# Kernel tuning notes

Measured on AMD Instinct MI355X. Metric: run time of the kernel, lower is better.

The kernel has to match this reference:

```python
import jax, jax.numpy as jnp
import numpy as np

D_IN = 1024
D_OUT = 1024
NUM_HEADS = 16
HEAD_DIM = D_OUT // NUM_HEADS


def setup_inputs() -> dict:
    key = jax.random.key(0)
    ks = jax.random.split(key, 6)
    B, S = 2, 2048
    scale = 1.0 / np.sqrt(D_IN)
    x = jax.random.normal(ks[0], (B, S, D_IN), dtype=jnp.float32)
    # Linear weights stored torch-style as [out_features, in_features]
    Wq = jax.random.normal(ks[1], (D_OUT, D_IN), dtype=jnp.float32) * scale
    Wk = jax.random.normal(ks[2], (D_OUT, D_IN), dtype=jnp.float32) * scale
    Wv = jax.random.normal(ks[3], (D_OUT, D_IN), dtype=jnp.float32) * scale
    Wo = jax.random.normal(ks[4], (D_OUT, D_IN), dtype=jnp.float32) * scale
    bo = jax.random.normal(ks[5], (D_OUT,), dtype=jnp.float32) * 0.01
    return {"x": x, "Wq": Wq, "Wk": Wk, "Wv": Wv, "Wo": Wo, "bo": bo}


def reference(x, Wq, Wk, Wv, Wo, bo):
    B, S, _ = x.shape
    H, hd = NUM_HEADS, HEAD_DIM
    # QKV projections (qkv_bias=False), split into heads: [B, H, S, hd]
    q = (x @ Wq.T).reshape(B, S, H, hd).transpose(0, 2, 1, 3)
    k = (x @ Wk.T).reshape(B, S, H, hd).transpose(0, 2, 1, 3)
    v = (x @ Wv.T).reshape(B, S, H, hd).transpose(0, 2, 1, 3)
    # scaled causal attention scores [B, H, S, S]
    scores = jnp.einsum("bhqd,bhkd->bhqk", q, k) / jnp.sqrt(jnp.float32(hd))
    causal = jnp.tril(jnp.ones((S, S), dtype=bool))
    scores = jnp.where(causal, scores, jnp.finfo(scores.dtype).min)
    attn = jax.nn.softmax(scores, axis=-1)  # dropout p=0.0 -> identity
    ctx = jnp.einsum("bhqk,bhkd->bhqd", attn, v)  # [B, H, S, hd]
    ctx = ctx.transpose(0, 2, 1, 3).reshape(B, S, H * hd)
    return ctx @ Wo.T + bo
```

## Files before the change

kernel.cpp:

```cpp
#include <hip/hip_runtime.h>
#include <hip/hip_bf16.h>

#define AS1 __attribute__((address_space(1)))
#define AS3 __attribute__((address_space(3)))

typedef __attribute__((ext_vector_type(4))) float floatx4;
typedef __attribute__((ext_vector_type(8))) short bf16x8;
typedef unsigned short u16;
typedef unsigned int u32;

__device__ __forceinline__ u16 f2b(float f) {
  u32 u = __builtin_bit_cast(u32, f);
  u += 0x7fffu + ((u >> 16) & 1u);
  return (u16)(u >> 16);
}
__device__ __forceinline__ u32 pk2(float lo, float hi) {
  __hip_bfloat162 h = __float22bfloat162_rn(float2{lo, hi});
  u32 u;
  __builtin_memcpy(&u, &h, 4);
  return u;
}
__device__ __forceinline__ bf16x8 cvt8(float4 a, float4 b) {
  uint4 u{pk2(a.x, a.y), pk2(a.z, a.w), pk2(b.x, b.y), pk2(b.z, b.w)};
  return __builtin_bit_cast(bf16x8, u);
}

__device__ __forceinline__ void gld16(const void* g, AS3 u32* l) {
  __builtin_amdgcn_global_load_lds((const AS1 u32*)(const AS1 void*)g, l, 16,
                                   0, 0);
}

#define QSCALE 0.18033688011112042f
#define QSHIFT 14.4269504088896f

__global__ __launch_bounds__(256) void cvt_all(
    const float* __restrict__ x, const float* __restrict__ wq,
    const float* __restrict__ wk, const float* __restrict__ wv,
    const float* __restrict__ wo, u16* __restrict__ xb, u16* __restrict__ wqb,
    u16* __restrict__ wkb, u16* __restrict__ wvb, u16* __restrict__ wob) {
  const int i = blockIdx.x * 256 + threadIdx.x;
  const float* src;
  u16* dst;
  int off;
  if (i < 524288) {
    src = x; dst = xb; off = i;
  } else {
    const int j = i - 524288;
    const int wsel = j >> 17;
    off = j & 131071;
    src = (wsel == 0) ? wq : (wsel == 1) ? wk : (wsel == 2) ? wv : wo;
    dst = (wsel == 0) ? wqb : (wsel == 1) ? wkb : (wsel == 2) ? wvb : wob;
  }
  const float4* p = (const float4*)(src + (size_t)off * 8);
  *(bf16x8*)(dst + (size_t)off * 8) = cvt8(p[0], p[1]);
}

__device__ __forceinline__ void gemm_bf16(const u16* __restrict__ A,
                                          const u16* __restrict__ B, short* sA,
                                          short* sB, floatx4 acc[4][4]) {
  const int tid = threadIdx.x;
  const int lane = tid & 63;
  const int w = tid >> 6;
  const int l15 = lane & 15, quad = lane >> 4;
  const int wm = w >> 1, wn = w & 1;

  const u16* ga = A + ((size_t)(w * 32 + (lane >> 2))) * 1024 + (lane & 3) * 8;
  const u16* gb = B + ((size_t)(w * 32 + (lane >> 2))) * 1024 + (lane & 3) * 8;
  AS3 u32* la = (AS3 u32*)(AS3 short*)sA + w * 512;
  AS3 u32* lb = (AS3 u32*)(AS3 short*)sB + w * 512;

  for (int kt = 0; kt < 32; ++kt) {
    __syncthreads();
    gld16(ga, la);
    gld16(ga + (size_t)16 * 1024, la + 256);
    gld16(gb, lb);
    gld16(gb + (size_t)16 * 1024, lb + 256);
    ga += 32;
    gb += 32;
    __syncthreads();

    bf16x8 af[4], bfr[4];
#pragma unroll
    for (int mc = 0; mc < 4; ++mc)
      af[mc] = *(const bf16x8*)&sA[(wm * 64 + mc * 16 + l15) * 32 + quad * 8];
#pragma unroll
    for (int nc = 0; nc < 4; ++nc)
      bfr[nc] = *(const bf16x8*)&sB[(wn * 64 + nc * 16 + l15) * 32 + quad * 8];
#pragma unroll
    for (int mc = 0; mc < 4; ++mc)
#pragma unroll
      for (int nc = 0; nc < 4; ++nc)
        acc[mc][nc] = __builtin_amdgcn_mfma_f32_16x16x32_bf16(
            af[mc], bfr[nc], acc[mc][nc], 0, 0, 0);
  }
}

__device__ __forceinline__ void qkv_epilogue(floatx4 acc[4][4], int m0, int nb,
                                             int sel, u16* __restrict__ Q,
                                             u16* __restrict__ K,
                                             u16* __restrict__ Vt) {
  const int tid = threadIdx.x;
  const int lane = tid & 63, w = tid >> 6;
  const int l15 = lane & 15, quad = lane >> 4;
  const int wm = w >> 1, wn = w & 1;
#pragma unroll
  for (int mc = 0; mc < 4; ++mc) {
#pragma unroll
    for (int nc = 0; nc < 4; ++nc) {
      const int nn = nb + wn * 64 + nc * 16 + l15;
      const int h = nn >> 6, d = nn & 63;
#pragma unroll
      for (int r = 0; r < 4; ++r) {
        const int m = m0 + wm * 64 + mc * 16 + quad * 4 + r;
        const int b = m >> 11, s = m & 2047;
        const int bh = b * 16 + h;
        float av = acc[mc][nc][r];
        if (sel == 0) av *= QSCALE;
        const u16 v = f2b(av);
        if (sel == 0)
          Q[((size_t)bh * 2048 + s) * 64 + d] = v;
        else if (sel == 1)
          K[((size_t)bh * 2048 + s) * 64 + d] = v;
        else
          Vt[((size_t)bh * 64 + d) * 2048 + s] = v;
      }
    }
  }
}

__global__ __launch_bounds__(256) void qkv_gemm_b(
    const u16* __restrict__ xb, const u16* __restrict__ Wqb,
    const u16* __restrict__ Wkb, const u16* __restrict__ Wvb,
    u16* __restrict__ Q, u16* __restrict__ K, u16* __restrict__ Vt) {
  __shared__ __align__(16) short smem[2 * 128 * 32];
  const int m0 = blockIdx.x * 128;
  const int by = blockIdx.y;
  const int sel = by >> 3;
  const int nb = (by & 7) * 128;
  const u16* W = (sel == 0) ? Wqb : (sel == 1) ? Wkb : Wvb;

  floatx4 acc[4][4];
#pragma unroll
  for (int i = 0; i < 4; i++)
#pragma unroll
    for (int j = 0; j < 4; j++) acc[i][j] = (floatx4)0.0f;
  gemm_bf16(xb + (size_t)m0 * 1024, W + (size_t)nb * 1024, smem,
            smem + 128 * 32, acc);
  qkv_epilogue(acc, m0, nb, sel, Q, K, Vt);
}

__global__ __launch_bounds__(256) void out_gemm_b(const u16* __restrict__ ctx,
                                                  const u16* __restrict__ Wob,
                                                  const float* __restrict__ bo,
                                                  float* __restrict__ out) {
  __shared__ __align__(16) short smem[128 * 32 + 64 * 32];
  const int tid = threadIdx.x;
  const int lane = tid & 63, w = tid >> 6;
  const int l15 = lane & 15, quad = lane >> 4;
  const int m0 = blockIdx.x * 128;
  const int n0 = blockIdx.y * 64;
  short* sA = smem;
  short* sB = smem + 128 * 32;

  const u16* ga = ctx + ((size_t)(m0 + w * 32 + (lane >> 2))) * 1024 +
                  (lane & 3) * 8;
  const u16* gb = Wob + ((size_t)(n0 + w * 16 + (lane >> 2))) * 1024 +
                  (lane & 3) * 8;
  AS3 u32* la = (AS3 u32*)(AS3 short*)sA + w * 512;
  AS3 u32* lb = (AS3 u32*)(AS3 short*)sB + w * 256;

  floatx4 acc[2][4];
#pragma unroll
  for (int i = 0; i < 2; i++)
#pragma unroll
    for (int j = 0; j < 4; j++) acc[i][j] = (floatx4)0.0f;

  for (int kt = 0; kt < 32; ++kt) {
    __syncthreads();
    gld16(ga, la);
    gld16(ga + (size_t)16 * 1024, la + 256);
    gld16(gb, lb);
    ga += 32;
    gb += 32;
    __syncthreads();

    bf16x8 af[2], bfr[4];
#pragma unroll
    for (int mc = 0; mc < 2; ++mc)
      af[mc] = *(const bf16x8*)&sA[(w * 32 + mc * 16 + l15) * 32 + quad * 8];
#pragma unroll
    for (int nc = 0; nc < 4; ++nc)
      bfr[nc] = *(const bf16x8*)&sB[(nc * 16 + l15) * 32 + quad * 8];
#pragma unroll
    for (int mc = 0; mc < 2; ++mc)
#pragma unroll
      for (int nc = 0; nc < 4; ++nc)
        acc[mc][nc] = __builtin_amdgcn_mfma_f32_16x16x32_bf16(
            af[mc], bfr[nc], acc[mc][nc], 0, 0, 0);
  }

#pragma unroll
  for (int mc = 0; mc < 2; ++mc)
#pragma unroll
    for (int nc = 0; nc < 4; ++nc) {
      const int n = n0 + nc * 16 + l15;
      const float bias = bo[n];
#pragma unroll
      for (int r = 0; r < 4; ++r) {
        const int m = m0 + w * 32 + mc * 16 + quad * 4 + r;
        out[(size_t)m * 1024 + n] = acc[mc][nc][r] + bias;
      }
    }
}

template <bool F32A>
__device__ __forceinline__ void gemm128(const void* __restrict__ A,
                                        const float* __restrict__ B, short* sA,
                                        short* sB, floatx4 acc[4][4]) {
  const int tid = threadIdx.x;
  const int lane = tid & 63;
  const int w = tid >> 6;
  const int l15 = lane & 15, quad = lane >> 4;
  const int wm = w >> 1, wn = w & 1;
  const int srow = tid >> 1;
  const int scb = (tid & 1) * 16;

  float4 pa[4], pb[4];
  int4 pa16[2];
  if constexpr (F32A) {
    const float* ap = (const float*)A + (size_t)srow * 1024 + scb;
    pa[0] = ((const float4*)ap)[0]; pa[1] = ((const float4*)ap)[1];
    pa[2] = ((const float4*)ap)[2]; pa[3] = ((const float4*)ap)[3];
  } else {
    const u16* ap = (const u16*)A + (size_t)srow * 1024 + scb;
    pa16[0] = ((const int4*)ap)[0]; pa16[1] = ((const int4*)ap)[1];
  }
  {
    const float* bp = B + (size_t)srow * 1024 + scb;
    pb[0] = ((const float4*)bp)[0]; pb[1] = ((const float4*)bp)[1];
    pb[2] = ((const float4*)bp)[2]; pb[3] = ((const float4*)bp)[3];
  }

  for (int kt = 0; kt < 32; ++kt) {
    __syncthreads();
    if constexpr (F32A) {
      *(bf16x8*)&sA[srow * 40 + scb] = cvt8(pa[0], pa[1]);
      *(bf16x8*)&sA[srow * 40 + scb + 8] = cvt8(pa[2], pa[3]);
    } else {
      *(int4*)&sA[srow * 40 + scb] = pa16[0];
      *(int4*)&sA[srow * 40 + scb + 8] = pa16[1];
    }
    *(bf16x8*)&sB[srow * 40 + scb] = cvt8(pb[0], pb[1]);
    *(bf16x8*)&sB[srow * 40 + scb + 8] = cvt8(pb[2], pb[3]);
    __syncthreads();

    if (kt < 31) {
      const int k0 = (kt + 1) * 32;
      if constexpr (F32A) {
        const float* ap = (const float*)A + (size_t)srow * 1024 + k0 + scb;
        pa[0] = ((const float4*)ap)[0]; pa[1] = ((const float4*)ap)[1];
        pa[2] = ((const float4*)ap)[2]; pa[3] = ((const float4*)ap)[3];
      } else {
        const u16* ap = (const u16*)A + (size_t)srow * 1024 + k0 + scb;
        pa16[0] = ((const int4*)ap)[0]; pa16[1] = ((const int4*)ap)[1];
      }
      const float* bp = B + (size_t)srow * 1024 + k0 + scb;
      pb[0] = ((const float4*)bp)[0]; pb[1] = ((const float4*)bp)[1];
      pb[2] = ((const float4*)bp)[2]; pb[3] = ((const float4*)bp)[3];
    }

    bf16x8 af[4], bfr[4];
#pragma unroll
    for (int mc = 0; mc < 4; ++mc)
      af[mc] = *(const bf16x8*)&sA[(wm * 64 + mc * 16 + l15) * 40 + quad * 8];
#pragma unroll
    for (int nc = 0; nc < 4; ++nc)
      bfr[nc] = *(const bf16x8*)&sB[(wn * 64 + nc * 16 + l15) * 40 + quad * 8];
#pragma unroll
    for (int mc = 0; mc < 4; ++mc)
#pragma unroll
      for (int nc = 0; nc < 4; ++nc)
        acc[mc][nc] = __builtin_amdgcn_mfma_f32_16x16x32_bf16(
            af[mc], bfr[nc], acc[mc][nc], 0, 0, 0);
  }
}

__global__ __launch_bounds__(256) void qkv_gemm_f(
    const float* __restrict__ x, const float* __restrict__ Wq,
    const float* __restrict__ Wk, const float* __restrict__ Wv,
    u16* __restrict__ Q, u16* __restrict__ K, u16* __restrict__ Vt) {
  __shared__ __align__(16) short smem[2 * 128 * 40];
  const int m0 = blockIdx.x * 128;
  const int by = blockIdx.y;
  const int sel = by >> 3;
  const int nb = (by & 7) * 128;
  const float* W = (sel == 0) ? Wq : (sel == 1) ? Wk : Wv;

  floatx4 acc[4][4];
#pragma unroll
  for (int i = 0; i < 4; i++)
#pragma unroll
    for (int j = 0; j < 4; j++) acc[i][j] = (floatx4)0.0f;
  gemm128<true>((const void*)(x + (size_t)m0 * 1024), W + (size_t)nb * 1024,
                smem, smem + 128 * 40, acc);
  qkv_epilogue(acc, m0, nb, sel, Q, K, Vt);
}

__global__ __launch_bounds__(256) void out_gemm_f(const u16* __restrict__ ctx,
                                                  const float* __restrict__ Wo,
                                                  const float* __restrict__ bo,
                                                  float* __restrict__ out) {
  __shared__ __align__(16) short smem[2 * 128 * 40];
  const int tid = threadIdx.x;
  const int lane = tid & 63, w = tid >> 6;
  const int l15 = lane & 15, quad = lane >> 4;
  const int wm = w >> 1, wn = w & 1;
  const int m0 = blockIdx.x * 128;
  const int n0 = blockIdx.y * 128;

  floatx4 acc[4][4];
#pragma unroll
  for (int i = 0; i < 4; i++)
#pragma unroll
    for (int j = 0; j < 4; j++) acc[i][j] = (floatx4)0.0f;
  gemm128<false>((const void*)(ctx + (size_t)m0 * 1024),
                 Wo + (size_t)n0 * 1024, smem, smem + 128 * 40, acc);

#pragma unroll
  for (int mc = 0; mc < 4; ++mc)
#pragma unroll
    for (int nc = 0; nc < 4; ++nc) {
      const int n = n0 + wn * 64 + nc * 16 + l15;
      const float bias = bo[n];
#pragma unroll
      for (int r = 0; r < 4; ++r) {
        const int m = m0 + wm * 64 + mc * 16 + quad * 4 + r;
        out[(size_t)m * 1024 + n] = acc[mc][nc][r] + bias;
      }
    }
}

template <bool CLEAN>
__device__ __forceinline__ void attn_tile(const u16* __restrict__ sKb,
                                          const u16* __restrict__ sVb,
                                          const int l15, const int quad,
                                          const int jbase, const int wrow,
                                          const bf16x8 aQ0, const bf16x8 aQ1,
                                          floatx4 (&acc)[4], floatx4& lsv) {
  if constexpr (CLEAN) {
    bf16x8 ka[2][4];
    uint2 va[2][8];
#pragma unroll
    for (int u = 0; u < 4; ++u) {
      const u16* kp0 = sKb + l15 * 72 + quad * 8;
      ka[0][u] = *(const bf16x8*)(kp0 + (u >> 1) * (16 * 72) + (u & 1) * 32);
    }
#pragma unroll
    for (int dt = 0; dt < 4; ++dt) {
      const u16* vp = sVb + (dt * 16 + l15) * 136 + quad * 4;
      va[0][2 * dt] = *(const uint2*)(vp);
      va[0][2 * dt + 1] = *(const uint2*)(vp + 16);
    }
#pragma unroll
    for (int kp = 0; kp < 4; ++kp) {
      const int pc = kp & 1, pn = (kp + 1) & 1;
      if (kp < 3) {
        const u16* kp1 = sKb + ((kp + 1) * 32 + l15) * 72 + quad * 8;
#pragma unroll
        for (int u = 0; u < 4; ++u)
          ka[pn][u] =
              *(const bf16x8*)(kp1 + (u >> 1) * (16 * 72) + (u & 1) * 32);
#pragma unroll
        for (int dt = 0; dt < 4; ++dt) {
          const u16* vp =
              sVb + (dt * 16 + l15) * 136 + (kp + 1) * 32 + quad * 4;
          va[pn][2 * dt] = *(const uint2*)(vp);
          va[pn][2 * dt + 1] = *(const uint2*)(vp + 16);
        }
      }
      floatx4 st0 = (floatx4)0.0f, st1 = (floatx4)0.0f;
      __builtin_amdgcn_s_setprio(1);
      st0 = __builtin_amdgcn_mfma_f32_16x16x32_bf16(ka[pc][0], aQ0, st0, 0, 0,
                                                    0);
      st1 = __builtin_amdgcn_mfma_f32_16x16x32_bf16(ka[pc][2], aQ0, st1, 0, 0,
                                                    0);
      st0 = __builtin_amdgcn_mfma_f32_16x16x32_bf16(ka[pc][1], aQ1, st0, 0, 0,
                                                    0);
      st1 = __builtin_amdgcn_mfma_f32_16x16x32_bf16(ka[pc][3], aQ1, st1, 0, 0,
                                                    0);
      __builtin_amdgcn_s_setprio(0);
      float p0[4], p1[4];
#pragma unroll
      for (int r = 0; r < 4; ++r) {
        p0[r] = __builtin_amdgcn_exp2f(st0[r] - QSHIFT);
        p1[r] = __builtin_amdgcn_exp2f(st1[r] - QSHIFT);
      }
#pragma unroll
      for (int r = 0; r < 4; ++r) lsv[r] += p0[r] + p1[r];
      uint4 pfu{pk2(p0[0], p0[1]), pk2(p0[2], p0[3]), pk2(p1[0], p1[1]),
                pk2(p1[2], p1[3])};
      const bf16x8 pf8 = __builtin_bit_cast(bf16x8, pfu);
      __builtin_amdgcn_s_setprio(1);
#pragma unroll
      for (int dt = 0; dt < 4; ++dt) {
        uint4 avu{va[pc][2 * dt].x, va[pc][2 * dt].y, va[pc][2 * dt + 1].x,
                  va[pc][2 * dt + 1].y};
        bf16x8 av8 = __builtin_bit_cast(bf16x8, avu);
        acc[dt] = __builtin_amdgcn_mfma_f32_16x16x32_bf16(av8, pf8, acc[dt],
                                                          0, 0, 0);
      }
      __builtin_amdgcn_s_setprio(0);
    }
  } else {
#pragma unroll 2
    for (int kp = 0; kp < 4; ++kp) {
      const int kbase = jbase + kp * 32;
      if (kbase > wrow + 15) break;

      const u16* kr0 = sKb + (kp * 32 + l15) * 72 + quad * 8;
      bf16x8 ak00 = *(const bf16x8*)(kr0);
      bf16x8 ak01 = *(const bf16x8*)(kr0 + 32);
      floatx4 st0 = (floatx4)0.0f;
      st0 = __builtin_amdgcn_mfma_f32_16x16x32_bf16(ak00, aQ0, st0, 0, 0, 0);
      st0 = __builtin_amdgcn_mfma_f32_16x16x32_bf16(ak01, aQ1, st0, 0, 0, 0);

      const bool have1 = (kbase + 16 <= wrow + 15);
      floatx4 st1 = (floatx4)0.0f;
      if (have1) {
        const u16* kr1 = kr0 + 16 * 72;
        bf16x8 ak10 = *(const bf16x8*)(kr1);
        bf16x8 ak11 = *(const bf16x8*)(kr1 + 32);
        st1 = __builtin_amdgcn_mfma_f32_16x16x32_bf16(ak10, aQ0, st1, 0, 0, 0);
        st1 = __builtin_amdgcn_mfma_f32_16x16x32_bf16(ak11, aQ1, st1, 0, 0, 0);
      }

      float p0[4], p1[4];
      const bool m0b = (kbase + 15 > wrow);
#pragma unroll
      for (int r = 0; r < 4; ++r) {
        float t = st0[r] - QSHIFT;
        if (m0b && (kbase + quad * 4 + r > wrow + l15)) t = -1e30f;
        p0[r] = __builtin_amdgcn_exp2f(t);
      }
      if (have1) {
        const bool m1b = (kbase + 31 > wrow);
#pragma unroll
        for (int r = 0; r < 4; ++r) {
          float t = st1[r] - QSHIFT;
          if (m1b && (kbase + 16 + quad * 4 + r > wrow + l15)) t = -1e30f;
          p1[r] = __builtin_amdgcn_exp2f(t);
        }
      } else {
        p1[0] = p1[1] = p1[2] = p1[3] = 0.0f;
      }
#pragma unroll
      for (int r = 0; r < 4; ++r) lsv[r] += p0[r] + p1[r];

      uint4 pfu{pk2(p0[0], p0[1]), pk2(p0[2], p0[3]), pk2(p1[0], p1[1]),
                pk2(p1[2], p1[3])};
      const bf16x8 pf8 = __builtin_bit_cast(bf16x8, pfu);

#pragma unroll
      for (int dt = 0; dt < 4; ++dt) {
        const u16* vp = sVb + (dt * 16 + l15) * 136 + kp * 32 + quad * 4;
        uint2 v0 = *(const uint2*)(vp);
        uint2 v1 = *(const uint2*)(vp + 16);
        uint4 avu{v0.x, v0.y, v1.x, v1.y};
        bf16x8 av8 = __builtin_bit_cast(bf16x8, avu);
        acc[dt] = __builtin_amdgcn_mfma_f32_16x16x32_bf16(av8, pf8, acc[dt],
                                                          0, 0, 0);
      }
    }
  }
}

__device__ __forceinline__ void attn_write(u16* tw, const floatx4 (&acc)[4],
                                           const floatx4 lsv, const int l15,
                                           const int quad, const int wrow,
                                           const int b, const int h,
                                           u16* __restrict__ ctx) {
  float lsum = (lsv[0] + lsv[1]) + (lsv[2] + lsv[3]);
  lsum += __shfl_xor(lsum, 16, 64);
  lsum += __shfl_xor(lsum, 32, 64);
  const float inv = 1.0f / lsum;
#pragma unroll
  for (int dt = 0; dt < 4; ++dt) {
    uint2 o2{pk2(acc[dt][0] * inv, acc[dt][1] * inv),
             pk2(acc[dt][2] * inv, acc[dt][3] * inv)};
    *(uint2*)&tw[l15 * 72 + dt * 16 + quad * 4] = o2;
  }
  bf16x8 o0 = *(const bf16x8*)&tw[l15 * 72 + quad * 16];
  bf16x8 o1 = *(const bf16x8*)&tw[l15 * 72 + quad * 16 + 8];
  u16* cp =
      ctx + ((size_t)(b * 2048 + wrow + l15)) * 1024 + h * 64 + quad * 16;
  *(bf16x8*)cp = o0;
  *(bf16x8*)(cp + 8) = o1;
}

__global__ __launch_bounds__(512, 4) void attn_kernel(
    const u16* __restrict__ Q, const u16* __restrict__ K,
    const u16* __restrict__ Vt, u16* __restrict__ ctx) {
  const int bid = blockIdx.x;
  const int s = bid >> 5;
  const int bh = bid & 31;
  const int c = (s < 8) ? (15 - s) : (s - 8);
  const int tid = threadIdx.x;
  const int w = tid >> 6;
  const int lane = tid & 63;
  const int l15 = lane & 15;
  const int quad = lane >> 4;

  constexpr int KE = 128 * 72;
  constexpr int VE = 64 * 136;
  constexpr int BUF = KE + VE;
  __shared__ __align__(16) u16 lds[2 * BUF];

  const int kr = tid >> 2, kc = (tid & 3) * 16;
  const int vd = tid >> 3, vc = (tid & 7) * 16;
  const int b = bh >> 4, h = bh & 15;

  const u16* Kg = K + (size_t)bh * 2048 * 64;
  const u16* Vg = Vt + (size_t)bh * 64 * 2048;

  const int wrow = c * 128 + w * 16;

  bf16x8 aQ0, aQ1;
  {
    const u16* qp = Q + ((size_t)bh * 2048 + wrow + l15) * 64 + quad * 8;
    aQ0 = *(const bf16x8*)(qp);
    aQ1 = *(const bf16x8*)(qp + 32);
  }

  floatx4 acc[4];
#pragma unroll
  for (int i = 0; i < 4; ++i) acc[i] = (floatx4)0.0f;
  floatx4 lsv = (floatx4)0.0f;

  int4 pk[2], pv[2];
  pk[0] = *(const int4*)(Kg + (size_t)kr * 64 + kc);
  pk[1] = *(const int4*)(Kg + (size_t)kr * 64 + kc + 8);
  pv[0] = *(const int4*)(Vg + (size_t)vd * 2048 + vc);
  pv[1] = *(const int4*)(Vg + (size_t)vd * 2048 + vc + 8);
  *(int4*)&lds[kr * 72 + kc] = pk[0];
  *(int4*)&lds[kr * 72 + kc + 8] = pk[1];
  *(int4*)&lds[KE + vd * 136 + vc] = pv[0];
  *(int4*)&lds[KE + vd * 136 + vc + 8] = pv[1];
  __syncthreads();
  int cur = 0;

  for (int jb = 0; jb <= c; ++jb) {
    const u16* sKb = lds + cur * BUF;
    const u16* sVb = sKb + KE;

    const int jn = (jb < c) ? (jb + 1) * 128 : -1;
    if (jn >= 0) {
      pk[0] = *(const int4*)(Kg + (size_t)(jn + kr) * 64 + kc);
      pk[1] = *(const int4*)(Kg + (size_t)(jn + kr) * 64 + kc + 8);
      pv[0] = *(const int4*)(Vg + (size_t)vd * 2048 + jn + vc);
      pv[1] = *(const int4*)(Vg + (size_t)vd * 2048 + jn + vc + 8);
    }

    const int jbase = jb * 128;
    if (jb < c)
      attn_tile<true>(sKb, sVb, l15, quad, jbase, wrow, aQ0, aQ1, acc, lsv);
    else
      attn_tile<false>(sKb, sVb, l15, quad, jbase, wrow, aQ0, aQ1, acc, lsv);

    if (jn >= 0) {
      u16* dK = lds + (cur ^ 1) * BUF;
      u16* dV = dK + KE;
      *(int4*)&dK[kr * 72 + kc] = pk[0];
      *(int4*)&dK[kr * 72 + kc + 8] = pk[1];
      *(int4*)&dV[vd * 136 + vc] = pv[0];
      *(int4*)&dV[vd * 136 + vc + 8] = pv[1];
    }
    __syncthreads();
    cur ^= 1;
  }

  u16* tw = lds + (cur ^ 1) * BUF + (w * 16) * 72;
  attn_write(tw, acc, lsv, l15, quad, wrow, b, h, ctx);
}

extern "C" void kernel_launch(void* const* d_in, const int* in_sizes, int n_in,
                              void* d_out, int out_size, void* d_ws,
                              size_t ws_size, hipStream_t stream) {
  const float* x = (const float*)d_in[0];
  const float* Wq = (const float*)d_in[1];
  const float* Wk = (const float*)d_in[2];
  const float* Wv = (const float*)d_in[3];
  const float* Wo = (const float*)d_in[4];
  const float* bo = (const float*)d_in[5];
  float* out = (float*)d_out;

  u16* Q = (u16*)d_ws;
  u16* K = Q + (size_t)4096 * 1024;
  u16* Vt = K + (size_t)4096 * 1024;
  u16* ctx = Vt + (size_t)4096 * 1024;

  if (ws_size >= (size_t)40 * 1024 * 1024) {
    u16* xb = ctx;
    u16* Wqb = (u16*)d_ws + (size_t)16 * 1024 * 1024;
    u16* Wkb = Wqb + (size_t)1024 * 1024;
    u16* Wvb = Wkb + (size_t)1024 * 1024;
    u16* Wob = Wvb + (size_t)1024 * 1024;

    cvt_all<<<4096, 256, 0, stream>>>(x, Wq, Wk, Wv, Wo, xb, Wqb, Wkb, Wvb,
                                      Wob);
    qkv_gemm_b<<<dim3(32, 24), 256, 0, stream>>>(xb, Wqb, Wkb, Wvb, Q, K, Vt);
    attn_kernel<<<512, 512, 0, stream>>>(Q, K, Vt, ctx);
    out_gemm_b<<<dim3(32, 16), 256, 0, stream>>>(ctx, Wob, bo, out);
  } else {
    qkv_gemm_f<<<dim3(32, 24), 256, 0, stream>>>(x, Wq, Wk, Wv, Q, K, Vt);
    attn_kernel<<<512, 512, 0, stream>>>(Q, K, Vt, ctx);
    out_gemm_f<<<dim3(32, 8), 256, 0, stream>>>(ctx, Wo, bo, out);
  }
}
```

Before: 198.4 us.

## Process two 16-row query blocks per wave in attention to reuse K/V fragments

The attention kernel now uses 256 threads (4 waves) per block, each wave handling 32 query rows instead of 16. K and V fragments loaded from LDS are reused across two query sub-tiles, which halves LDS reads per MFMA. Each thread loads more of the K/V tile per step. The cost is higher register pressure, since accumulators and score fragments double, and fewer waves per block for hiding latency. Launch bounds change to (256,2).

```diff
diff --git a/kernel.cpp b/kernel.cpp
--- a/kernel.cpp
+++ b/kernel.cpp
@@ -340,137 +340,157 @@
     }
 }
 
-template <bool CLEAN>
-__device__ __forceinline__ void attn_tile(const u16* __restrict__ sKb,
-                                          const u16* __restrict__ sVb,
-                                          const int l15, const int quad,
-                                          const int jbase, const int wrow,
-                                          const bf16x8 aQ0, const bf16x8 aQ1,
-                                          floatx4 (&acc)[4], floatx4& lsv) {
-  if constexpr (CLEAN) {
-    bf16x8 ka[2][4];
-    uint2 va[2][8];
-#pragma unroll
-    for (int u = 0; u < 4; ++u) {
-      const u16* kp0 = sKb + l15 * 72 + quad * 8;
-      ka[0][u] = *(const bf16x8*)(kp0 + (u >> 1) * (16 * 72) + (u & 1) * 32);
-    }
+__device__ __forceinline__ void attn_tile_masked(
+    const u16* __restrict__ sKb, const u16* __restrict__ sVb, const int l15,
+    const int quad, const int jbase, const int wrow, const bf16x8 aQ0,
+    const bf16x8 aQ1, floatx4 (&acc)[4], floatx4& lsv) {
+#pragma unroll 2
+  for (int kp = 0; kp < 4; ++kp) {
+    const int kbase = jbase + kp * 32;
+    if (kbase > wrow + 15) break;
+
+    const u16* kr0 = sKb + (kp * 32 + l15) * 72 + quad * 8;
+    bf16x8 ak00 = *(const bf16x8*)(kr0);
+    bf16x8 ak01 = *(const bf16x8*)(kr0 + 32);
+    floatx4 st0 = (floatx4)0.0f;
+    st0 = __builtin_amdgcn_mfma_f32_16x16x32_bf16(ak00, aQ0, st0, 0, 0, 0);
+    st0 = __builtin_amdgcn_mfma_f32_16x16x32_bf16(ak01, aQ1, st0, 0, 0, 0);
+
+    const bool have1 = (kbase + 16 <= wrow + 15);
+    floatx4 st1 = (floatx4)0.0f;
+    if (have1) {
+      const u16* kr1 = kr0 + 16 * 72;
+      bf16x8 ak10 = *(const bf16x8*)(kr1);
+      bf16x8 ak11 = *(const bf16x8*)(kr1 + 32);
+      st1 = __builtin_amdgcn_mfma_f32_16x16x32_bf16(ak10, aQ0, st1, 0, 0, 0);
+      st1 = __builtin_amdgcn_mfma_f32_16x16x32_bf16(ak11, aQ1, st1, 0, 0, 0);
+    }
+
+    float p0[4], p1[4];
+    const bool m0b = (kbase + 15 > wrow);
+#pragma unroll
+    for (int r = 0; r < 4; ++r) {
+      float t = st0[r] - QSHIFT;
+      if (m0b && (kbase + quad * 4 + r > wrow + l15)) t = -1e30f;
+      p0[r] = __builtin_amdgcn_exp2f(t);
+    }
+    if (have1) {
+      const bool m1b = (kbase + 31 > wrow);
+#pragma unroll
+      for (int r = 0; r < 4; ++r) {
+        float t = st1[r] - QSHIFT;
+        if (m1b && (kbase + 16 + quad * 4 + r > wrow + l15)) t = -1e30f;
+        p1[r] = __builtin_amdgcn_exp2f(t);
+      }
+    } else {
+      p1[0] = p1[1] = p1[2] = p1[3] = 0.0f;
+    }
+#pragma unroll
+    for (int r = 0; r < 4; ++r) lsv[r] += p0[r] + p1[r];
+
+    uint4 pfu{pk2(p0[0], p0[1]), pk2(p0[2], p0[3]), pk2(p1[0], p1[1]),
+              pk2(p1[2], p1[3])};
+    const bf16x8 pf8 = __builtin_bit_cast(bf16x8, pfu);
+
 #pragma unroll
     for (int dt = 0; dt < 4; ++dt) {
-      const u16* vp = sVb + (dt * 16 + l15) * 136 + quad * 4;
-      va[0][2 * dt] = *(const uint2*)(vp);
-      va[0][2 * dt + 1] = *(const uint2*)(vp + 16);
-    }
-#pragma unroll
-    for (int kp = 0; kp < 4; ++kp) {
-      const int pc = kp & 1, pn = (kp + 1) & 1;
-      if (kp < 3) {
-        const u16* kp1 = sKb + ((kp + 1) * 32 + l15) * 72 + quad * 8;
-#pragma unroll
-        for (int u = 0; u < 4; ++u)
-          ka[pn][u] =
-              *(const bf16x8*)(kp1 + (u >> 1) * (16 * 72) + (u & 1) * 32);
-#pragma unroll
-        for (int dt = 0; dt < 4; ++dt) {
-          const u16* vp =
-              sVb + (dt * 16 + l15) * 136 + (kp + 1) * 32 + quad * 4;
-          va[pn][2 * dt] = *(const uint2*)(vp);
-          va[pn][2 * dt + 1] = *(const uint2*)(vp + 16);
-        }
-      }
-      floatx4 st0 = (floatx4)0.0f, st1 = (floatx4)0.0f;
-      __builtin_amdgcn_s_setprio(1);
-      st0 = __builtin_amdgcn_mfma_f32_16x16x32_bf16(ka[pc][0], aQ0, st0, 0, 0,
-                                                    0);
-      st1 = __builtin_amdgcn_mfma_f32_16x16x32_bf16(ka[pc][2], aQ0, st1, 0, 0,
-                                                    0);
-      st0 = __builtin_amdgcn_mfma_f32_16x16x32_bf16(ka[pc][1], aQ1, st0, 0, 0,
-                                                    0);
-      st1 = __builtin_amdgcn_mfma_f32_16x16x32_bf16(ka[pc][3], aQ1, st1, 0, 0,
-                                                    0);
-      __builtin_amdgcn_s_setprio(0);
-      float p0[4], p1[4];
-#pragma unroll
-      for (int r = 0; r < 4; ++r) {
-        p0[r] = __builtin_amdgcn_exp2f(st0[r] - QSHIFT);
-        p1[r] = __builtin_amdgcn_exp2f(st1[r] - QSHIFT);
-      }
-#pragma unroll
-      for (int r = 0; r < 4; ++r) lsv[r] += p0[r] + p1[r];
-      uint4 pfu{pk2(p0[0], p0[1]), pk2(p0[2], p0[3]), pk2(p1[0], p1[1]),
-                pk2(p1[2], p1[3])};
-      const bf16x8 pf8 = __builtin_bit_cast(bf16x8, pfu);
-      __builtin_amdgcn_s_setprio(1);
+      const u16* vp = sVb + (dt * 16 + l15) * 136 + kp * 32 + quad * 4;
+      uint2 v0 = *(const uint2*)(vp);
+      uint2 v1 = *(const uint2*)(vp + 16);
+      uint4 avu{v0.x, v0.y, v1.x, v1.y};
+      bf16x8 av8 = __builtin_bit_cast(bf16x8, avu);
+      acc[dt] = __builtin_amdgcn_mfma_f32_16x16x32_bf16(av8, pf8, acc[dt], 0,
+                                                        0, 0);
+    }
+  }
+}
+
+__device__ __forceinline__ void attn_tile2_clean(
+    const u16* __restrict__ sKb, const u16* __restrict__ sVb, const int l15,
+    const int quad, const bf16x8 aQ00, const bf16x8 aQ01, const bf16x8 aQ10,
+    const bf16x8 aQ11, floatx4 (&acc0)[4], floatx4 (&acc1)[4], floatx4& lsv0,
+    floatx4& lsv1) {
+  bf16x8 ka[2][4];
+  uint2 va[2][8];
+#pragma unroll
+  for (int u = 0; u < 4; ++u) {
+    const u16* kp0 = sKb + l15 * 72 + quad * 8;
+    ka[0][u] = *(const bf16x8*)(kp0 + (u >> 1) * (16 * 72) + (u & 1) * 32);
+  }
+#pragma unroll
+  for (int dt = 0; dt < 4; ++dt) {
+    const u16* vp = sVb + (dt * 16 + l15) * 136 + quad * 4;
+    va[0][2 * dt] = *(const uint2*)(vp);
+    va[0][2 * dt + 1] = *(const uint2*)(vp + 16);
+  }
+#pragma unroll
+  for (int kp = 0; kp < 4; ++kp) {
+    const int pc = kp & 1, pn = (kp + 1) & 1;
+    if (kp < 3) {
+      const u16* kp1 = sKb + ((kp + 1) * 32 + l15) * 72 + quad * 8;
+#pragma unroll
+      for (int u = 0; u < 4; ++u)
+        ka[pn][u] = *(const bf16x8*)(kp1 + (u >> 1) * (16 * 72) + (u & 1) * 32);
 #pragma unroll
       for (int dt = 0; dt < 4; ++dt) {
-        uint4 avu{va[pc][2 * dt].x, va[pc][2 * dt].y, va[pc][2 * dt + 1].x,
-                  va[pc][2 * dt + 1].y};
-        bf16x8 av8 = __builtin_bit_cast(bf16x8, avu);
-        acc[dt] = __builtin_amdgcn_mfma_f32_16x16x32_bf16(av8, pf8, acc[dt],
-                                                          0, 0, 0);
-      }
-      __builtin_amdgcn_s_setprio(0);
-    }
-  } else {
-#pragma unroll 2
-    for (int kp = 0; kp < 4; ++kp) {
-      const int kbase = jbase + kp * 32;
-      if (kbase > wrow + 15) break;
-
-      const u16* kr0 = sKb + (kp * 32 + l15) * 72 + quad * 8;
-      bf16x8 ak00 = *(const bf16x8*)(kr0);
-      bf16x8 ak01 = *(const bf16x8*)(kr0 + 32);
-      floatx4 st0 = (floatx4)0.0f;
-      st0 = __builtin_amdgcn_mfma_f32_16x16x32_bf16(ak00, aQ0, st0, 0, 0, 0);
-      st0 = __builtin_amdgcn_mfma_f32_16x16x32_bf16(ak01, aQ1, st0, 0, 0, 0);
-
-      const bool have1 = (kbase + 16 <= wrow + 15);
-      floatx4 st1 = (floatx4)0.0f;
-      if (have1) {
-        const u16* kr1 = kr0 + 16 * 72;
-        bf16x8 ak10 = *(const bf16x8*)(kr1);
-        bf16x8 ak11 = *(const bf16x8*)(kr1 + 32);
-        st1 = __builtin_amdgcn_mfma_f32_16x16x32_bf16(ak10, aQ0, st1, 0, 0, 0);
-        st1 = __builtin_amdgcn_mfma_f32_16x16x32_bf16(ak11, aQ1, st1, 0, 0, 0);
-      }
-
-      float p0[4], p1[4];
-      const bool m0b = (kbase + 15 > wrow);
-#pragma unroll
-      for (int r = 0; r < 4; ++r) {
-        float t = st0[r] - QSHIFT;
-        if (m0b && (kbase + quad * 4 + r > wrow + l15)) t = -1e30f;
-        p0[r] = __builtin_amdgcn_exp2f(t);
-      }
-      if (have1) {
-        const bool m1b = (kbase + 31 > wrow);
-#pragma unroll
-        for (int r = 0; r < 4; ++r) {
-          float t = st1[r] - QSHIFT;
-          if (m1b && (kbase + 16 + quad * 4 + r > wrow + l15)) t = -1e30f;
-          p1[r] = __builtin_amdgcn_exp2f(t);
-        }
-      } else {
-        p1[0] = p1[1] = p1[2] = p1[3] = 0.0f;
-      }
-#pragma unroll
-      for (int r = 0; r < 4; ++r) lsv[r] += p0[r] + p1[r];
-
-      uint4 pfu{pk2(p0[0], p0[1]), pk2(p0[2], p0[3]), pk2(p1[0], p1[1]),
-                pk2(p1[2], p1[3])};
-      const bf16x8 pf8 = __builtin_bit_cast(bf16x8, pfu);
-
-#pragma unroll
-      for (int dt = 0; dt < 4; ++dt) {
-        const u16* vp = sVb + (dt * 16 + l15) * 136 + kp * 32 + quad * 4;
-        uint2 v0 = *(const uint2*)(vp);
-        uint2 v1 = *(const uint2*)(vp + 16);
-        uint4 avu{v0.x, v0.y, v1.x, v1.y};
-        bf16x8 av8 = __builtin_bit_cast(bf16x8, avu);
-        acc[dt] = __builtin_amdgcn_mfma_f32_16x16x32_bf16(av8, pf8, acc[dt],
-                                                          0, 0, 0);
-      }
-    }
+        const u16* vp = sVb + (dt * 16 + l15) * 136 + (kp + 1) * 32 + quad * 4;
+        va[pn][2 * dt] = *(const uint2*)(vp);
+        va[pn][2 * dt + 1] = *(const uint2*)(vp + 16);
+      }
+    }
+    floatx4 sa0 = (floatx4)0.0f, sa1 = (floatx4)0.0f;
+    floatx4 sb0 = (floatx4)0.0f, sb1 = (floatx4)0.0f;
+    __builtin_amdgcn_s_setprio(1);
+    sa0 = __builtin_amdgcn_mfma_f32_16x16x32_bf16(ka[pc][0], aQ00, sa0, 0, 0,
+                                                  0);
+    sa1 = __builtin_amdgcn_mfma_f32_16x16x32_bf16(ka[pc][2], aQ00, sa1, 0, 0,
+                                                  0);
+    sb0 = __builtin_amdgcn_mfma_f32_16x16x32_bf16(ka[pc][0], aQ10, sb0, 0, 0,
+                                                  0);
+    sb1 = __builtin_amdgcn_mfma_f32_16x16x32_bf16(ka[pc][2], aQ10, sb1, 0, 0,
+                                                  0);
+    sa0 = __builtin_amdgcn_mfma_f32_16x16x32_bf16(ka[pc][1], aQ01, sa0, 0, 0,
+                                                  0);
+    sa1 = __builtin_amdgcn_mfma_f32_16x16x32_bf16(ka[pc][3], aQ01, sa1, 0, 0,
+                                                  0);
+    sb0 = __builtin_amdgcn_mfma_f32_16x16x32_bf16(ka[pc][1], aQ11, sb0, 0, 0,
+                                                  0);
+    sb1 = __builtin_amdgcn_mfma_f32_16x16x32_bf16(ka[pc][3], aQ11, sb1, 0, 0,
+                                                  0);
+    __builtin_amdgcn_s_setprio(0);
+
+    float pa0[4], pa1[4], pb0[4], pb1[4];
+#pragma unroll
+    for (int r = 0; r < 4; ++r) {
+      pa0[r] = __builtin_amdgcn_exp2f(sa0[r] - QSHIFT);
+      pa1[r] = __builtin_amdgcn_exp2f(sa1[r] - QSHIFT);
+      pb0[r] = __builtin_amdgcn_exp2f(sb0[r] - QSHIFT);
+      pb1[r] = __builtin_amdgcn_exp2f(sb1[r] - QSHIFT);
+    }
+#pragma unroll
+    for (int r = 0; r < 4; ++r) {
+      lsv0[r] += pa0[r] + pa1[r];
+      lsv1[r] += pb0[r] + pb1[r];
+    }
+    uint4 pfuA{pk2(pa0[0], pa0[1]), pk2(pa0[2], pa0[3]), pk2(pa1[0], pa1[1]),
+               pk2(pa1[2], pa1[3])};
+    uint4 pfuB{pk2(pb0[0], pb0[1]), pk2(pb0[2], pb0[3]), pk2(pb1[0], pb1[1]),
+               pk2(pb1[2], pb1[3])};
+    const bf16x8 pf8A = __builtin_bit_cast(bf16x8, pfuA);
+    const bf16x8 pf8B = __builtin_bit_cast(bf16x8, pfuB);
+
+    __builtin_amdgcn_s_setprio(1);
+#pragma unroll
+    for (int dt = 0; dt < 4; ++dt) {
+      uint4 avu{va[pc][2 * dt].x, va[pc][2 * dt].y, va[pc][2 * dt + 1].x,
+                va[pc][2 * dt + 1].y};
+      bf16x8 av8 = __builtin_bit_cast(bf16x8, avu);
+      acc0[dt] = __builtin_amdgcn_mfma_f32_16x16x32_bf16(av8, pf8A, acc0[dt],
+                                                         0, 0, 0);
+      acc1[dt] = __builtin_amdgcn_mfma_f32_16x16x32_bf16(av8, pf8B, acc1[dt],
+                                                         0, 0, 0);
+    }
+    __builtin_amdgcn_s_setprio(0);
   }
 }
 
@@ -497,7 +517,7 @@
   *(bf16x8*)(cp + 8) = o1;
 }
 
-__global__ __launch_bounds__(512, 4) void attn_kernel(
+__global__ __launch_bounds__(256, 2) void attn_kernel(
     const u16* __restrict__ Q, const u16* __restrict__ K,
     const u16* __restrict__ Vt, u16* __restrict__ ctx) {
   const int bid = blockIdx.x;
@@ -515,36 +535,44 @@
   constexpr int BUF = KE + VE;
   __shared__ __align__(16) u16 lds[2 * BUF];
 
-  const int kr = tid >> 2, kc = (tid & 3) * 16;
-  const int vd = tid >> 3, vc = (tid & 7) * 16;
+  const int kr = tid >> 1, kc = (tid & 1) * 32;
+  const int vd = tid >> 2, vc = (tid & 3) * 32;
   const int b = bh >> 4, h = bh & 15;
 
   const u16* Kg = K + (size_t)bh * 2048 * 64;
   const u16* Vg = Vt + (size_t)bh * 64 * 2048;
 
-  const int wrow = c * 128 + w * 16;
-
-  bf16x8 aQ0, aQ1;
+  const int wrow = c * 128 + w * 32;
+
+  bf16x8 aQ00, aQ01, aQ10, aQ11;
   {
-    const u16* qp = Q + ((size_t)bh * 2048 + wrow + l15) * 64 + quad * 8;
-    aQ0 = *(const bf16x8*)(qp);
-    aQ1 = *(const bf16x8*)(qp + 32);
-  }
-
-  floatx4 acc[4];
-#pragma unroll
-  for (int i = 0; i < 4; ++i) acc[i] = (floatx4)0.0f;
-  floatx4 lsv = (floatx4)0.0f;
-
-  int4 pk[2], pv[2];
-  pk[0] = *(const int4*)(Kg + (size_t)kr * 64 + kc);
-  pk[1] = *(const int4*)(Kg + (size_t)kr * 64 + kc + 8);
-  pv[0] = *(const int4*)(Vg + (size_t)vd * 2048 + vc);
-  pv[1] = *(const int4*)(Vg + (size_t)vd * 2048 + vc + 8);
-  *(int4*)&lds[kr * 72 + kc] = pk[0];
-  *(int4*)&lds[kr * 72 + kc + 8] = pk[1];
-  *(int4*)&lds[KE + vd * 136 + vc] = pv[0];
-  *(int4*)&lds[KE + vd * 136 + vc + 8] = pv[1];
+    const u16* q0 = Q + ((size_t)bh * 2048 + wrow + l15) * 64 + quad * 8;
+    aQ00 = *(const bf16x8*)(q0);
+    aQ01 = *(const bf16x8*)(q0 + 32);
+    const u16* q1 = Q + ((size_t)bh * 2048 + wrow + 16 + l15) * 64 + quad * 8;
+    aQ10 = *(const bf16x8*)(q1);
+    aQ11 = *(const bf16x8*)(q1 + 32);
+  }
+
+  floatx4 acc0[4], acc1[4];
+#pragma unroll
+  for (int i = 0; i < 4; ++i) {
+    acc0[i] = (floatx4)0.0f;
+    acc1[i] = (floatx4)0.0f;
+  }
+  floatx4 lsv0 = (floatx4)0.0f, lsv1 = (floatx4)0.0f;
+
+  int4 pk[4], pv[4];
+#pragma unroll
+  for (int i = 0; i < 4; ++i) {
+    pk[i] = *(const int4*)(Kg + (size_t)kr * 64 + kc + i * 8);
+    pv[i] = *(const int4*)(Vg + (size_t)vd * 2048 + vc + i * 8);
+  }
+#pragma unroll
+  for (int i = 0; i < 4; ++i) {
+    *(int4*)&lds[kr * 72 + kc + i * 8] = pk[i];
+    *(int4*)&lds[KE + vd * 136 + vc + i * 8] = pv[i];
+  }
   __syncthreads();
   int cur = 0;
 
@@ -554,32 +582,40 @@
 
     const int jn = (jb < c) ? (jb + 1) * 128 : -1;
     if (jn >= 0) {
-      pk[0] = *(const int4*)(Kg + (size_t)(jn + kr) * 64 + kc);
-      pk[1] = *(const int4*)(Kg + (size_t)(jn + kr) * 64 + kc + 8);
-      pv[0] = *(const int4*)(Vg + (size_t)vd * 2048 + jn + vc);
-      pv[1] = *(const int4*)(Vg + (size_t)vd * 2048 + jn + vc + 8);
+#pragma unroll
+      for (int i = 0; i < 4; ++i) {
+        pk[i] = *(const int4*)(Kg + (size_t)(jn + kr) * 64 + kc + i * 8);
+        pv[i] = *(const int4*)(Vg + (size_t)vd * 2048 + jn + vc + i * 8);
+      }
     }
 
     const int jbase = jb * 128;
-    if (jb < c)
-      attn_tile<true>(sKb, sVb, l15, quad, jbase, wrow, aQ0, aQ1, acc, lsv);
-    else
-      attn_tile<false>(sKb, sVb, l15, quad, jbase, wrow, aQ0, aQ1, acc, lsv);
+    if (jb < c) {
+      attn_tile2_clean(sKb, sVb, l15, quad, aQ00, aQ01, aQ10, aQ11, acc0,
+                       acc1, lsv0, lsv1);
+    } else {
+      attn_tile_masked(sKb, sVb, l15, quad, jbase, wrow, aQ00, aQ01, acc0,
+                       lsv0);
+      attn_tile_masked(sKb, sVb, l15, quad, jbase, wrow + 16, aQ10, aQ11,
+                       acc1, lsv1);
+    }
 
     if (jn >= 0) {
       u16* dK = lds + (cur ^ 1) * BUF;
       u16* dV = dK + KE;
-      *(int4*)&dK[kr * 72 + kc] = pk[0];
-      *(int4*)&dK[kr * 72 + kc + 8] = pk[1];
-      *(int4*)&dV[vd * 136 + vc] = pv[0];
-      *(int4*)&dV[vd * 136 + vc + 8] = pv[1];
+#pragma unroll
+      for (int i = 0; i < 4; ++i) {
+        *(int4*)&dK[kr * 72 + kc + i * 8] = pk[i];
+        *(int4*)&dV[vd * 136 + vc + i * 8] = pv[i];
+      }
     }
     __syncthreads();
     cur ^= 1;
   }
 
-  u16* tw = lds + (cur ^ 1) * BUF + (w * 16) * 72;
-  attn_write(tw, acc, lsv, l15, quad, wrow, b, h, ctx);
+  u16* tw = lds + (cur ^ 1) * BUF + (w * 32) * 72;
+  attn_write(tw, acc0, lsv0, l15, quad, wrow, b, h, ctx);
+  attn_write(tw + 16 * 72, acc1, lsv1, l15, quad, wrow + 16, b, h, ctx);
 }
 
 extern "C" void kernel_launch(void* const* d_in, const int* in_sizes, int n_in,
@@ -608,11 +644,11 @@
     cvt_all<<<4096, 256, 0, stream>>>(x, Wq, Wk, Wv, Wo, xb, Wqb, Wkb, Wvb,
                                       Wob);
     qkv_gemm_b<<<dim3(32, 24), 256, 0, stream>>>(xb, Wqb, Wkb, Wvb, Q, K, Vt);
-    attn_kernel<<<512, 512, 0, stream>>>(Q, K, Vt, ctx);
+    attn_kernel<<<512, 256, 0, stream>>>(Q, K, Vt, ctx);
     out_gemm_b<<<dim3(32, 16), 256, 0, stream>>>(ctx, Wob, bo, out);
   } else {
     qkv_gemm_f<<<dim3(32, 24), 256, 0, stream>>>(x, Wq, Wk, Wv, Q, K, Vt);
-    attn_kernel<<<512, 512, 0, stream>>>(Q, K, Vt, ctx);
+    attn_kernel<<<512, 256, 0, stream>>>(Q, K, Vt, ctx);
     out_gemm_f<<<dim3(32, 8), 256, 0, stream>>>(ctx, Wo, bo, out);
   }
 }
```

Measured after the change: 205.0 us. 1.03x slower.
